# Kernel tuning notes

Measured on AMD Instinct MI355X. Metric: run time of the kernel, lower is better.

The kernel has to match this reference:

```python
import jax, jax.numpy as jnp
import numpy as np

VTH = 0.5      # SNNParameters.vth_init
TAU = 0.25     # SNNParameters.tau_mem
_GAUSS_C = 1.0 / np.sqrt(0.3 * np.pi)  # surrogate-grad scale (unused in fwd)


def _heaviside(v):
    return (v > 0).astype(v.dtype)


def setup_inputs() -> dict:
    key = jax.random.key(0)
    x = jax.random.normal(key, (16, 128, 512, 32), dtype=jnp.float32)
    return {"x": x}


def reference(x):
    # x: [..., T]; LIF recurrence over the last (time) axis.
    xT = jnp.moveaxis(x, -1, 0)  # [T, ...]
    u0 = jnp.zeros(x.shape[:-1], dtype=x.dtype)
    o0 = jnp.zeros(x.shape[:-1], dtype=x.dtype)

    def step(carry, x_t):
        u, o_prev = carry
        u = TAU * u * (1.0 - o_prev) + x_t          # leaky integrate w/ reset
        o = _heaviside(u - VTH)                     # fire
        return (u, o), o

    _, outT = jax.lax.scan(step, (u0, o0), xT)
    return jnp.moveaxis(outT, 0, -1)  # back to [..., T]
```

## Files before the change

kernel.cpp:

```cpp
#include <hip/hip_runtime.h>


constexpr int T = 32;
constexpr float TAU = 0.25f;
constexpr float VTH = 0.5f;

__global__ __launch_bounds__(256) void LIFSpike_kernel(
    const float* __restrict__ x, float* __restrict__ out, int n_neurons) {
    int i = blockIdx.x * blockDim.x + threadIdx.x;
    if (i >= n_neurons) return;

    const float4* __restrict__ xp = reinterpret_cast<const float4*>(x) + (size_t)i * (T / 4);
    float4* __restrict__ op = reinterpret_cast<float4*>(out) + (size_t)i * (T / 4);

    float4 buf[T / 4];
#pragma unroll
    for (int j = 0; j < T / 4; ++j) buf[j] = xp[j];

    float u = 0.0f, o = 0.0f;
#pragma unroll
    for (int j = 0; j < T / 4; ++j) {
        float xs0 = buf[j].x, xs1 = buf[j].y, xs2 = buf[j].z, xs3 = buf[j].w;
        float4 r;

        u = TAU * u * (1.0f - o) + xs0;
        o = (u > VTH) ? 1.0f : 0.0f;
        r.x = o;

        u = TAU * u * (1.0f - o) + xs1;
        o = (u > VTH) ? 1.0f : 0.0f;
        r.y = o;

        u = TAU * u * (1.0f - o) + xs2;
        o = (u > VTH) ? 1.0f : 0.0f;
        r.z = o;

        u = TAU * u * (1.0f - o) + xs3;
        o = (u > VTH) ? 1.0f : 0.0f;
        r.w = o;

        op[j] = r;
    }
}

extern "C" void kernel_launch(void* const* d_in, const int* in_sizes, int n_in,
                              void* d_out, int out_size, void* d_ws, size_t ws_size,
                              hipStream_t stream) {
    const float* x = (const float*)d_in[0];
    float* out = (float*)d_out;
    int n_neurons = in_sizes[0] / T;
    int block = 256;
    int grid = (n_neurons + block - 1) / block;
    LIFSpike_kernel<<<grid, block, 0, stream>>>(x, out, n_neurons);
}
```

Before: 239.1 us.

## Stage input and output through swizzled LDS tile for coalesced global access

```diff
diff --git a/kernel.cpp b/kernel.cpp
--- a/kernel.cpp
+++ b/kernel.cpp
@@ -4,42 +4,58 @@
 constexpr int T = 32;
 constexpr float TAU = 0.25f;
 constexpr float VTH = 0.5f;
+constexpr int QUADS_PER_ROW = T / 4;
+constexpr int TILE_F4 = 256 * QUADS_PER_ROW;
+
+__device__ __forceinline__ int swz(int s) { return s ^ ((s >> 3) & 7); }
 
 __global__ __launch_bounds__(256) void LIFSpike_kernel(
-    const float* __restrict__ x, float* __restrict__ out, int n_neurons) {
-    int i = blockIdx.x * blockDim.x + threadIdx.x;
-    if (i >= n_neurons) return;
+    const float* __restrict__ x, float* __restrict__ out) {
+    __shared__ float4 tile[TILE_F4];
 
-    const float4* __restrict__ xp = reinterpret_cast<const float4*>(x) + (size_t)i * (T / 4);
-    float4* __restrict__ op = reinterpret_cast<float4*>(out) + (size_t)i * (T / 4);
+    const int t = threadIdx.x;
+    const size_t base = (size_t)blockIdx.x * TILE_F4;
 
-    float4 buf[T / 4];
+    const float4* __restrict__ xp = reinterpret_cast<const float4*>(x);
 #pragma unroll
-    for (int j = 0; j < T / 4; ++j) buf[j] = xp[j];
+    for (int k = 0; k < QUADS_PER_ROW; ++k) {
+        int s = k * 256 + t;
+        tile[swz(s)] = xp[base + s];
+    }
+    __syncthreads();
 
     float u = 0.0f, o = 0.0f;
 #pragma unroll
-    for (int j = 0; j < T / 4; ++j) {
-        float xs0 = buf[j].x, xs1 = buf[j].y, xs2 = buf[j].z, xs3 = buf[j].w;
+    for (int j = 0; j < QUADS_PER_ROW; ++j) {
+        int phys = t * QUADS_PER_ROW + (j ^ (t & 7));
+        float4 v = tile[phys];
         float4 r;
 
-        u = TAU * u * (1.0f - o) + xs0;
+        u = TAU * u * (1.0f - o) + v.x;
         o = (u > VTH) ? 1.0f : 0.0f;
         r.x = o;
 
-        u = TAU * u * (1.0f - o) + xs1;
+        u = TAU * u * (1.0f - o) + v.y;
         o = (u > VTH) ? 1.0f : 0.0f;
         r.y = o;
 
-        u = TAU * u * (1.0f - o) + xs2;
+        u = TAU * u * (1.0f - o) + v.z;
         o = (u > VTH) ? 1.0f : 0.0f;
         r.z = o;
 
-        u = TAU * u * (1.0f - o) + xs3;
+        u = TAU * u * (1.0f - o) + v.w;
         o = (u > VTH) ? 1.0f : 0.0f;
         r.w = o;
 
-        op[j] = r;
+        tile[phys] = r;
+    }
+    __syncthreads();
+
+    float4* __restrict__ op = reinterpret_cast<float4*>(out);
+#pragma unroll
+    for (int k = 0; k < QUADS_PER_ROW; ++k) {
+        int s = k * 256 + t;
+        op[base + s] = tile[swz(s)];
     }
 }
 
@@ -48,8 +64,7 @@
                               hipStream_t stream) {
     const float* x = (const float*)d_in[0];
     float* out = (float*)d_out;
-    int n_neurons = in_sizes[0] / T;
-    int block = 256;
-    int grid = (n_neurons + block - 1) / block;
-    LIFSpike_kernel<<<grid, block, 0, stream>>>(x, out, n_neurons);
+    int total_f4 = in_sizes[0] / 4;
+    int grid = total_f4 / TILE_F4;
+    LIFSpike_kernel<<<grid, 256, 0, stream>>>(x, out);
 }
```

Measured after the change: 229.7 us. 1.04x faster.
